# Optimization experiments

Hardware: AMD Instinct MI355X
Metric: run time of the kernel (lower is better)

## Reference

```python
import jax, jax.numpy as jnp
import numpy as np

LN_EPS = 1e-5


def setup_inputs() -> dict:
    key = jax.random.key(0)
    k1, = jax.random.split(key, 1)
    B, C, H, W = 16, 512, 64, 64
    HW = H * W
    x = jax.random.normal(k1, (B, C, H, W), dtype=jnp.float32)
    gamma = jnp.ones((), dtype=jnp.float32)          # Scale(1) learnable scalar
    ln_weight = jnp.ones((HW,), dtype=jnp.float32)   # LayerNorm weight
    ln_bias = jnp.zeros((HW,), dtype=jnp.float32)    # LayerNorm bias
    return {"x": x, "gamma": gamma, "ln_weight": ln_weight, "ln_bias": ln_bias}


def reference(x, gamma, ln_weight, ln_bias):
    B, C, H, W = x.shape
    v = x.reshape(B, C, H * W)                       # [B, C, HW] (Q = K = V)
    energy = jnp.einsum('bcn,bdn->bcd', v, v)        # [B, C, C]
    attn = jax.nn.softmax(energy, axis=-1)
    out = jnp.einsum('bcd,bdn->bcn', attn, v)        # [B, C, HW]
    out = gamma * out + v                            # scale + residual
    # LayerNorm over last dim (HW), torch eps=1e-5
    mean = jnp.mean(out, axis=-1, keepdims=True)
    var = jnp.mean(jnp.square(out - mean), axis=-1, keepdims=True)
    out = (out - mean) * jax.lax.rsqrt(var + LN_EPS) * ln_weight + ln_bias
    return out.reshape(B, C, H, W)
```

## Files before the change

### kernel.cpp

```cpp
#include <hip/hip_runtime.h>
#include <hip/hip_bf16.h>

#define B_DIM 16
#define C_DIM 512
#define HW_DIM 4096
#define LN_EPS 1e-5f

using bf16 = __hip_bfloat16;
typedef __bf16 v8bf __attribute__((ext_vector_type(8)));
typedef float v4f __attribute__((ext_vector_type(4)));
typedef unsigned short v8us __attribute__((ext_vector_type(8)));
using gptr_t = const __attribute__((address_space(1))) void*;
using lptr_t = __attribute__((address_space(3))) void*;

__device__ __forceinline__ unsigned short f2bf(float f) {
  unsigned int u = __float_as_uint(f);
  u = (u + 0x7fffu + ((u >> 16) & 1u)) >> 16;
  return (unsigned short)u;
}
__device__ __forceinline__ float bf2f(unsigned short us) {
  return __uint_as_float(((unsigned int)us) << 16);
}

__global__ __launch_bounds__(256) void k_convert_transpose(
    const float* __restrict__ x, unsigned short* __restrict__ v,
    unsigned short* __restrict__ vt) {
  __shared__ unsigned short tile[64][66];
  const int tid = threadIdx.x;
  const int b = blockIdx.z;
  const int n0 = blockIdx.x * 64;
  const int c0 = blockIdx.y * 64;
  const size_t boff = (size_t)b * ((size_t)C_DIM * HW_DIM);
  const float* xb = x + boff;
  unsigned short* vb = v + boff;
  unsigned short* vtb = vt + boff;

  const int cl = tid >> 3;
  const int h8 = (tid & 7) * 8;
#pragma unroll
  for (int j = 0; j < 2; ++j) {
    const int c = cl + j * 32;
    const float* src = xb + (size_t)(c0 + c) * HW_DIM + n0 + h8;
    const float4 f0 = ((const float4*)src)[0];
    const float4 f1 = ((const float4*)src)[1];
    v8us pack;
    pack[0] = f2bf(f0.x); pack[1] = f2bf(f0.y);
    pack[2] = f2bf(f0.z); pack[3] = f2bf(f0.w);
    pack[4] = f2bf(f1.x); pack[5] = f2bf(f1.y);
    pack[6] = f2bf(f1.z); pack[7] = f2bf(f1.w);
    *(v8us*)(vb + (size_t)(c0 + c) * HW_DIM + n0 + h8) = pack;
#pragma unroll
    for (int e = 0; e < 8; ++e) tile[c][h8 + e] = pack[e];
  }
  __syncthreads();
  const int nl = tid >> 3;
  const int c8 = (tid & 7) * 8;
#pragma unroll
  for (int j = 0; j < 2; ++j) {
    const int n = nl + j * 32;
    v8us pack;
#pragma unroll
    for (int e = 0; e < 8; ++e) pack[e] = tile[c8 + e][n];
    *(v8us*)(vtb + (size_t)(n0 + n) * C_DIM + c0 + c8) = pack;
  }
}

__device__ __forceinline__ void stage_tiles(
    const bf16* __restrict__ a_base, const bf16* __restrict__ b_base,
    const int stride, const int k0, const int wave, const int lane,
    bf16* ldsA, bf16* ldsB) {
  const int srow = lane >> 3;
  const int skcol = (lane & 7) * 8;
#pragma unroll
  for (int i = 0; i < 4; ++i) {
    const int ci = wave * 4 + i;
    const int row = ci * 8 + srow;
    __builtin_amdgcn_global_load_lds(
        (gptr_t)(a_base + (size_t)row * stride + k0 + skcol),
        (lptr_t)(ldsA + ci * 512), 16, 0, 0);
    __builtin_amdgcn_global_load_lds(
        (gptr_t)(b_base + (size_t)row * stride + k0 + skcol),
        (lptr_t)(ldsB + ci * 512), 16, 0, 0);
  }
}

__device__ __forceinline__ void compute_tile(
    const bf16* ldsA, const bf16* ldsB, const int wave, const int lane,
    v4f acc[4][4]) {
  const int kb = (lane >> 4) * 8;
  const int rl = lane & 15;
  const int wr = wave >> 1, wc = wave & 1;
#pragma unroll
  for (int kk = 0; kk < 2; ++kk) {
    v8bf af[4], bfr[4];
#pragma unroll
    for (int m = 0; m < 4; ++m)
      af[m] = *(const v8bf*)(ldsA + (wr * 64 + m * 16 + rl) * 64 + kk * 32 + kb);
#pragma unroll
    for (int n = 0; n < 4; ++n)
      bfr[n] = *(const v8bf*)(ldsB + (wc * 64 + n * 16 + rl) * 64 + kk * 32 + kb);
#pragma unroll
    for (int m = 0; m < 4; ++m)
#pragma unroll
      for (int n = 0; n < 4; ++n)
        acc[m][n] = __builtin_amdgcn_mfma_f32_16x16x32_bf16(af[m], bfr[n], acc[m][n], 0, 0, 0);
  }
}

__device__ __forceinline__ void gemm_dbuf_loop(
    const bf16* __restrict__ a_base, const bf16* __restrict__ b_base,
    const int stride, const int ksteps, const int wave, const int lane,
    bf16* ldsA0, bf16* ldsB0, bf16* ldsA1, bf16* ldsB1, v4f acc[4][4]) {
  stage_tiles(a_base, b_base, stride, 0, wave, lane, ldsA0, ldsB0);
  __syncthreads();
  int cur = 0;
  for (int kt = 0; kt < ksteps - 1; ++kt) {
    if (cur == 0)
      stage_tiles(a_base, b_base, stride, (kt + 1) * 64, wave, lane, ldsA1, ldsB1);
    else
      stage_tiles(a_base, b_base, stride, (kt + 1) * 64, wave, lane, ldsA0, ldsB0);
    compute_tile(cur == 0 ? ldsA0 : ldsA1, cur == 0 ? ldsB0 : ldsB1, wave, lane, acc);
    __syncthreads();
    cur ^= 1;
  }
  compute_tile(cur == 0 ? ldsA0 : ldsA1, cur == 0 ? ldsB0 : ldsB1, wave, lane, acc);
}

__global__ __launch_bounds__(256) void k_gemm1(
    const bf16* __restrict__ v, float* __restrict__ e_part) {
  __shared__ __align__(16) bf16 lds[4][128 * 64];
  int t = blockIdx.x;
  const int ks = t >> 8;
  t &= 255;
  const int b = t >> 4;
  const int cb = (t >> 2) & 3;
  const int db = t & 3;
  const int tid = threadIdx.x;
  const int wave = tid >> 6, lane = tid & 63;
  const bf16* vb = v + (size_t)b * ((size_t)C_DIM * HW_DIM) + ks * (HW_DIM / 2);
  v4f acc[4][4] = {};
  gemm_dbuf_loop(vb + (size_t)(cb * 128) * HW_DIM,
                 vb + (size_t)(db * 128) * HW_DIM,
                 HW_DIM, (HW_DIM / 2) / 64, wave, lane,
                 lds[0], lds[1], lds[2], lds[3], acc);
  float* eb = e_part + (size_t)ks * ((size_t)B_DIM * C_DIM * C_DIM) +
              (size_t)b * (C_DIM * C_DIM);
  const int wr = wave >> 1, wc = wave & 1;
  const int rl = lane & 15;
  const int r0 = (lane >> 4) * 4;
#pragma unroll
  for (int m = 0; m < 4; ++m)
#pragma unroll
    for (int n = 0; n < 4; ++n) {
      const int row0 = cb * 128 + wr * 64 + m * 16 + r0;
      const int col = db * 128 + wc * 64 + n * 16 + rl;
#pragma unroll
      for (int r = 0; r < 4; ++r)
        eb[(size_t)(row0 + r) * C_DIM + col] = acc[m][n][r];
    }
}

__global__ __launch_bounds__(256) void k_softmax(
    const float* __restrict__ e_part, unsigned short* __restrict__ attn) {
  const int row = blockIdx.x;
  const float* e0 = e_part + (size_t)row * C_DIM;
  const float* e1 = e0 + (size_t)B_DIM * C_DIM * C_DIM;
  const int tid = threadIdx.x;
  const float v0 = e0[tid] + e1[tid];
  const float v1 = e0[tid + 256] + e1[tid + 256];
  float mx = fmaxf(v0, v1);
#pragma unroll
  for (int off = 32; off > 0; off >>= 1) mx = fmaxf(mx, __shfl_xor(mx, off));
  __shared__ float rmax[4], rsum[4];
  const int wv = tid >> 6, ln = tid & 63;
  if (ln == 0) rmax[wv] = mx;
  __syncthreads();
  mx = fmaxf(fmaxf(rmax[0], rmax[1]), fmaxf(rmax[2], rmax[3]));
  const float p0 = __expf(v0 - mx), p1 = __expf(v1 - mx);
  float s = p0 + p1;
#pragma unroll
  for (int off = 32; off > 0; off >>= 1) s += __shfl_xor(s, off);
  if (ln == 0) rsum[wv] = s;
  __syncthreads();
  s = rsum[0] + rsum[1] + rsum[2] + rsum[3];
  const float inv = 1.0f / s;
  attn[(size_t)row * C_DIM + tid] = f2bf(p0 * inv);
  attn[(size_t)row * C_DIM + tid + 256] = f2bf(p1 * inv);
}

#define TILE_E (256 * 64)

__device__ __forceinline__ void stage_half8(
    const bf16* __restrict__ g, bf16* l, int k0, int wave, int lane) {
  const int lrow = lane >> 3, lc = lane & 7;
#pragma unroll
  for (int i = 0; i < 2; ++i) {
    const int row = i * 64 + wave * 8 + lrow;
    __builtin_amdgcn_global_load_lds(
        (gptr_t)(g + (size_t)row * C_DIM + k0 + ((lc ^ (row & 7)) << 3)),
        (lptr_t)(l + (i * 64 + wave * 8) * 64), 16, 0, 0);
  }
}
__device__ __forceinline__ void stage_op2(
    const bf16* __restrict__ g, bf16* l, int k0, int wave, int lane) {
  stage_half8(g, l, k0, wave, lane);
  stage_half8(g + (size_t)128 * C_DIM, l + 128 * 64, k0, wave, lane);
}
__device__ __forceinline__ v8bf ld_frag8(const bf16* l, int row, int j) {
  return *(const v8bf*)(l + row * 64 + ((j ^ (row & 7)) << 3));
}

__global__ __launch_bounds__(512, 2) void k_gemm2(
    const bf16* __restrict__ attn, const bf16* __restrict__ vt,
    const unsigned short* __restrict__ vres, const float* __restrict__ gamma,
    float* __restrict__ out) {
  __shared__ __align__(16) bf16 smA[2][TILE_E];
  __shared__ __align__(16) bf16 smB[2][TILE_E];
  const int bid = blockIdx.x;
  const int t = (bid & 7) * 64 + (bid >> 3);
  const int b = t >> 5;
  const int cb = (t >> 4) & 1;
  const int nb = t & 15;
  const int tid = threadIdx.x;
  const int wave = tid >> 6, lane = tid & 63;
  const int wm = wave >> 2, wn = wave & 3;
  const int rl = lane & 15, kq = lane >> 4;

  const bf16* Ab = attn + (size_t)b * (C_DIM * C_DIM) + (size_t)(cb * 256) * C_DIM;
  const bf16* Bb = vt + (size_t)b * ((size_t)C_DIM * HW_DIM) + (size_t)(nb * 256) * C_DIM;

  v4f acc[8][4] = {};

  stage_op2(Bb, smB[0], 0, wave, lane);
  stage_op2(Ab, smA[0], 0, wave, lane);
  stage_op2(Bb, smB[1], 64, wave, lane);
  stage_op2(Ab, smA[1], 64, wave, lane);
  asm volatile("s_waitcnt vmcnt(8)" ::: "memory");
  __builtin_amdgcn_s_barrier();

  v8bf a[4][2], b01[2][2], b23[2][2];
  for (int kt = 0; kt < 8; ++kt) {
    const bf16* LA = smA[kt & 1];
    const bf16* LB = smB[kt & 1];
#pragma unroll
    for (int mi = 0; mi < 4; ++mi)
#pragma unroll
      for (int kk = 0; kk < 2; ++kk)
        a[mi][kk] = ld_frag8(LA, wm * 128 + mi * 16 + rl, kk * 4 + kq);
#pragma unroll
    for (int ni = 0; ni < 2; ++ni)
#pragma unroll
      for (int kk = 0; kk < 2; ++kk)
        b01[ni][kk] = ld_frag8(LB, wn * 64 + ni * 16 + rl, kk * 4 + kq);
    __builtin_amdgcn_s_barrier();
    asm volatile("s_waitcnt lgkmcnt(0)");
    __builtin_amdgcn_s_setprio(1);
#pragma unroll
    for (int kk = 0; kk < 2; ++kk)
#pragma unroll
      for (int mi = 0; mi < 4; ++mi)
#pragma unroll
        for (int ni = 0; ni < 2; ++ni)
          acc[mi][ni] = __builtin_amdgcn_mfma_f32_16x16x32_bf16(
              a[mi][kk], b01[ni][kk], acc[mi][ni], 0, 0, 0);
    __builtin_amdgcn_s_setprio(0);
    __builtin_amdgcn_s_barrier();
#pragma unroll
    for (int ni = 0; ni < 2; ++ni)
#pragma unroll
      for (int kk = 0; kk < 2; ++kk)
        b23[ni][kk] = ld_frag8(LB, wn * 64 + (ni + 2) * 16 + rl, kk * 4 + kq);
    __builtin_amdgcn_s_barrier();
    asm volatile("s_waitcnt lgkmcnt(0)");
    __builtin_amdgcn_s_setprio(1);
#pragma unroll
    for (int kk = 0; kk < 2; ++kk)
#pragma unroll
      for (int mi = 0; mi < 4; ++mi)
#pragma unroll
        for (int ni = 0; ni < 2; ++ni)
          acc[mi][ni + 2] = __builtin_amdgcn_mfma_f32_16x16x32_bf16(
              a[mi][kk], b23[ni][kk], acc[mi][ni + 2], 0, 0, 0);
    __builtin_amdgcn_s_setprio(0);
    __builtin_amdgcn_s_barrier();
#pragma unroll
    for (int mi = 0; mi < 4; ++mi)
#pragma unroll
      for (int kk = 0; kk < 2; ++kk)
        a[mi][kk] = ld_frag8(LA, wm * 128 + (mi + 4) * 16 + rl, kk * 4 + kq);
    if (kt < 6) stage_op2(Bb, smB[kt & 1], (kt + 2) * 64, wave, lane);
    __builtin_amdgcn_s_barrier();
    asm volatile("s_waitcnt lgkmcnt(0)");
    __builtin_amdgcn_s_setprio(1);
#pragma unroll
    for (int kk = 0; kk < 2; ++kk)
#pragma unroll
      for (int mi = 0; mi < 4; ++mi)
#pragma unroll
        for (int ni = 0; ni < 2; ++ni)
          acc[mi + 4][ni + 2] = __builtin_amdgcn_mfma_f32_16x16x32_bf16(
              a[mi][kk], b23[ni][kk], acc[mi + 4][ni + 2], 0, 0, 0);
    __builtin_amdgcn_s_setprio(0);
    __builtin_amdgcn_s_barrier();
    if (kt < 6) stage_op2(Ab, smA[kt & 1], (kt + 2) * 64, wave, lane);
    __builtin_amdgcn_s_barrier();
    __builtin_amdgcn_s_setprio(1);
#pragma unroll
    for (int kk = 0; kk < 2; ++kk)
#pragma unroll
      for (int mi = 0; mi < 4; ++mi)
#pragma unroll
        for (int ni = 0; ni < 2; ++ni)
          acc[mi + 4][ni] = __builtin_amdgcn_mfma_f32_16x16x32_bf16(
              a[mi][kk], b01[ni][kk], acc[mi + 4][ni], 0, 0, 0);
    __builtin_amdgcn_s_setprio(0);
    if (kt < 6)
      asm volatile("s_waitcnt vmcnt(8)" ::: "memory");
    else if (kt == 6)
      asm volatile("s_waitcnt vmcnt(0)" ::: "memory");
    __builtin_amdgcn_s_barrier();
  }

  const float g = gamma[0];
  const size_t boff = (size_t)b * ((size_t)C_DIM * HW_DIM);
  const unsigned short* xb = vres + boff;
  float* ob = out + boff;
  const int r0 = kq * 4;
#pragma unroll
  for (int mi = 0; mi < 8; ++mi)
#pragma unroll
    for (int ni = 0; ni < 4; ++ni) {
      const int c0 = cb * 256 + wm * 128 + mi * 16 + r0;
      const int nn = nb * 256 + wn * 64 + ni * 16 + rl;
#pragma unroll
      for (int r = 0; r < 4; ++r) {
        const size_t idx = (size_t)(c0 + r) * HW_DIM + nn;
        ob[idx] = g * acc[mi][ni][r] + bf2f(xb[idx]);
      }
    }
}

__global__ __launch_bounds__(256) void k_ln(
    float* __restrict__ out, const float* __restrict__ w,
    const float* __restrict__ bias) {
  const int row = blockIdx.x;
  float* p = out + (size_t)row * HW_DIM;
  const int tid = threadIdx.x;
  float4 vals[4];
  float s = 0.f, ss = 0.f;
#pragma unroll
  for (int i = 0; i < 4; ++i) {
    const float4 vv = ((const float4*)p)[tid + i * 256];
    vals[i] = vv;
    s += vv.x + vv.y + vv.z + vv.w;
    ss += vv.x * vv.x + vv.y * vv.y + vv.z * vv.z + vv.w * vv.w;
  }
#pragma unroll
  for (int off = 32; off > 0; off >>= 1) {
    s += __shfl_xor(s, off);
    ss += __shfl_xor(ss, off);
  }
  __shared__ float rs[4], rss[4];
  const int wv = tid >> 6, ln = tid & 63;
  if (ln == 0) { rs[wv] = s; rss[wv] = ss; }
  __syncthreads();
  s = rs[0] + rs[1] + rs[2] + rs[3];
  ss = rss[0] + rss[1] + rss[2] + rss[3];
  const float mean = s * (1.f / HW_DIM);
  const float var = ss * (1.f / HW_DIM) - mean * mean;
  const float rstd = rsqrtf(var + LN_EPS);
#pragma unroll
  for (int i = 0; i < 4; ++i) {
    const int idx = tid + i * 256;
    const float4 vv = vals[i];
    const float4 w4 = ((const float4*)w)[idx];
    const float4 b4 = ((const float4*)bias)[idx];
    float4 r;
    r.x = (vv.x - mean) * rstd * w4.x + b4.x;
    r.y = (vv.y - mean) * rstd * w4.y + b4.y;
    r.z = (vv.z - mean) * rstd * w4.z + b4.z;
    r.w = (vv.w - mean) * rstd * w4.w + b4.w;
    ((float4*)p)[idx] = r;
  }
}

extern "C" void kernel_launch(void* const* d_in, const int* in_sizes, int n_in,
                              void* d_out, int out_size, void* d_ws, size_t ws_size,
                              hipStream_t stream) {
  const float* x = (const float*)d_in[0];
  const float* gamma = (const float*)d_in[1];
  const float* lnw = (const float*)d_in[2];
  const float* lnb = (const float*)d_in[3];
  float* out = (float*)d_out;
  char* ws = (char*)d_ws;

  const size_t n_elem = (size_t)B_DIM * C_DIM * HW_DIM;
  const size_t e_elems = (size_t)B_DIM * C_DIM * C_DIM;
  unsigned short* vbf = (unsigned short*)ws;
  unsigned short* vbfT = (unsigned short*)(ws + 2 * n_elem);
  float* e_part = (float*)(ws + 4 * n_elem);
  unsigned short* attn =
      (unsigned short*)(ws + 4 * n_elem + 2 * e_elems * sizeof(float));

  k_convert_transpose<<<dim3(HW_DIM / 64, C_DIM / 64, B_DIM), 256, 0, stream>>>(
      x, vbf, vbfT);
  k_gemm1<<<512, 256, 0, stream>>>((const bf16*)vbf, e_part);
  k_softmax<<<B_DIM * C_DIM, 256, 0, stream>>>(e_part, attn);
  k_gemm2<<<512, 512, 0, stream>>>((const bf16*)attn, (const bf16*)vbfT,
                                   vbf, gamma, out);
  k_ln<<<B_DIM * C_DIM, 256, 0, stream>>>(out, lnw, lnb);
}
```

Measured before the change: 231.0 us.

## Stage GEMM2 epilogue through LDS for coalesced stores; move residual into LayerNorm

The GEMM2 epilogue now writes accumulators into a merged, XOR-swizzled shared buffer in two halves, then writes full rows back with float4 coalesced stores instead of scattered scalar stores. The gamma scaling and bf16 residual add move from GEMM2 into the LayerNorm kernel, which already reads each row. This targets poor store coalescing in GEMM2 and removes its strided residual reads. The cost is extra barriers and LDS traffic in the epilogue, plus an extra bf16 read stream in LayerNorm.

```diff
diff --git a/kernel.cpp b/kernel.cpp
--- a/kernel.cpp
+++ b/kernel.cpp
@@ -10,6 +10,7 @@
 typedef __bf16 v8bf __attribute__((ext_vector_type(8)));
 typedef float v4f __attribute__((ext_vector_type(4)));
 typedef unsigned short v8us __attribute__((ext_vector_type(8)));
+typedef unsigned short v4us __attribute__((ext_vector_type(4)));
 using gptr_t = const __attribute__((address_space(1))) void*;
 using lptr_t = __attribute__((address_space(3))) void*;
 
@@ -212,10 +213,8 @@
 
 __global__ __launch_bounds__(512, 2) void k_gemm2(
     const bf16* __restrict__ attn, const bf16* __restrict__ vt,
-    const unsigned short* __restrict__ vres, const float* __restrict__ gamma,
     float* __restrict__ out) {
-  __shared__ __align__(16) bf16 smA[2][TILE_E];
-  __shared__ __align__(16) bf16 smB[2][TILE_E];
+  __shared__ __align__(16) bf16 smem[4 * TILE_E];
   const int bid = blockIdx.x;
   const int t = (bid & 7) * 64 + (bid >> 3);
   const int b = t >> 5;
@@ -231,17 +230,19 @@
 
   v4f acc[8][4] = {};
 
-  stage_op2(Bb, smB[0], 0, wave, lane);
-  stage_op2(Ab, smA[0], 0, wave, lane);
-  stage_op2(Bb, smB[1], 64, wave, lane);
-  stage_op2(Ab, smA[1], 64, wave, lane);
+  stage_op2(Bb, smem + 2 * TILE_E, 0, wave, lane);
+  stage_op2(Ab, smem, 0, wave, lane);
+  stage_op2(Bb, smem + 3 * TILE_E, 64, wave, lane);
+  stage_op2(Ab, smem + TILE_E, 64, wave, lane);
   asm volatile("s_waitcnt vmcnt(8)" ::: "memory");
   __builtin_amdgcn_s_barrier();
 
   v8bf a[4][2], b01[2][2], b23[2][2];
   for (int kt = 0; kt < 8; ++kt) {
-    const bf16* LA = smA[kt & 1];
-    const bf16* LB = smB[kt & 1];
+    const bf16* LA = smem + (kt & 1) * TILE_E;
+    const bf16* LB = smem + (2 + (kt & 1)) * TILE_E;
+    bf16* SA = smem + (kt & 1) * TILE_E;
+    bf16* SB = smem + (2 + (kt & 1)) * TILE_E;
 #pragma unroll
     for (int mi = 0; mi < 4; ++mi)
 #pragma unroll
@@ -288,7 +289,7 @@
 #pragma unroll
       for (int kk = 0; kk < 2; ++kk)
         a[mi][kk] = ld_frag8(LA, wm * 128 + (mi + 4) * 16 + rl, kk * 4 + kq);
-    if (kt < 6) stage_op2(Bb, smB[kt & 1], (kt + 2) * 64, wave, lane);
+    if (kt < 6) stage_op2(Bb, SB, (kt + 2) * 64, wave, lane);
     __builtin_amdgcn_s_barrier();
     asm volatile("s_waitcnt lgkmcnt(0)");
     __builtin_amdgcn_s_setprio(1);
@@ -302,7 +303,7 @@
               a[mi][kk], b23[ni][kk], acc[mi + 4][ni + 2], 0, 0, 0);
     __builtin_amdgcn_s_setprio(0);
     __builtin_amdgcn_s_barrier();
-    if (kt < 6) stage_op2(Ab, smA[kt & 1], (kt + 2) * 64, wave, lane);
+    if (kt < 6) stage_op2(Ab, SA, (kt + 2) * 64, wave, lane);
     __builtin_amdgcn_s_barrier();
     __builtin_amdgcn_s_setprio(1);
 #pragma unroll
@@ -321,36 +322,58 @@
     __builtin_amdgcn_s_barrier();
   }
 
-  const float g = gamma[0];
-  const size_t boff = (size_t)b * ((size_t)C_DIM * HW_DIM);
-  const unsigned short* xb = vres + boff;
-  float* ob = out + boff;
-  const int r0 = kq * 4;
-#pragma unroll
-  for (int mi = 0; mi < 8; ++mi)
-#pragma unroll
-    for (int ni = 0; ni < 4; ++ni) {
-      const int c0 = cb * 256 + wm * 128 + mi * 16 + r0;
-      const int nn = nb * 256 + wn * 64 + ni * 16 + rl;
-#pragma unroll
-      for (int r = 0; r < 4; ++r) {
-        const size_t idx = (size_t)(c0 + r) * HW_DIM + nn;
-        ob[idx] = g * acc[mi][ni][r] + bf2f(xb[idx]);
-      }
+  float* smf = (float*)smem;
+  float* ob = out + (size_t)b * ((size_t)C_DIM * HW_DIM) +
+              (size_t)(cb * 256) * HW_DIM + nb * 256;
+#pragma unroll
+  for (int h = 0; h < 2; ++h) {
+    if (wm == h) {
+#pragma unroll
+      for (int mi = 0; mi < 8; ++mi)
+#pragma unroll
+        for (int ni = 0; ni < 4; ++ni)
+#pragma unroll
+          for (int rr = 0; rr < 4; ++rr) {
+            const int rloc = mi * 16 + kq * 4 + rr;
+            const int col = wn * 64 + ni * 16 + rl;
+            const int key = rloc & 7;
+            smf[rloc * 256 + ((((col >> 2) ^ key) << 2) | (col & 3))] =
+                acc[mi][ni][rr];
+          }
     }
+    __syncthreads();
+#pragma unroll
+    for (int it = 0; it < 16; ++it) {
+      const int rloc = it * 8 + wave;
+      const float4 vv =
+          *(const float4*)(smf + rloc * 256 + ((lane ^ (rloc & 7)) << 2));
+      *(float4*)(ob + (size_t)(h * 128 + rloc) * HW_DIM + lane * 4) = vv;
+    }
+    __syncthreads();
+  }
 }
 
 __global__ __launch_bounds__(256) void k_ln(
-    float* __restrict__ out, const float* __restrict__ w,
+    float* __restrict__ out, const unsigned short* __restrict__ vres,
+    const float* __restrict__ gamma, const float* __restrict__ w,
     const float* __restrict__ bias) {
   const int row = blockIdx.x;
   float* p = out + (size_t)row * HW_DIM;
+  const unsigned short* vr = vres + (size_t)row * HW_DIM;
+  const float g = gamma[0];
   const int tid = threadIdx.x;
   float4 vals[4];
   float s = 0.f, ss = 0.f;
 #pragma unroll
   for (int i = 0; i < 4; ++i) {
-    const float4 vv = ((const float4*)p)[tid + i * 256];
+    const int idx = tid + i * 256;
+    const float4 av = ((const float4*)p)[idx];
+    const v4us rv = *(const v4us*)(vr + idx * 4);
+    float4 vv;
+    vv.x = g * av.x + bf2f(rv[0]);
+    vv.y = g * av.y + bf2f(rv[1]);
+    vv.z = g * av.z + bf2f(rv[2]);
+    vv.w = g * av.w + bf2f(rv[3]);
     vals[i] = vv;
     s += vv.x + vv.y + vv.z + vv.w;
     ss += vv.x * vv.x + vv.y * vv.y + vv.z * vv.z + vv.w * vv.w;
@@ -406,7 +429,6 @@
       x, vbf, vbfT);
   k_gemm1<<<512, 256, 0, stream>>>((const bf16*)vbf, e_part);
   k_softmax<<<B_DIM * C_DIM, 256, 0, stream>>>(e_part, attn);
-  k_gemm2<<<512, 512, 0, stream>>>((const bf16*)attn, (const bf16*)vbfT,
-                                   vbf, gamma, out);
-  k_ln<<<B_DIM * C_DIM, 256, 0, stream>>>(out, lnw, lnb);
-}
+  k_gemm2<<<512, 512, 0, stream>>>((const bf16*)attn, (const bf16*)vbfT, out);
+  k_ln<<<B_DIM * C_DIM, 256, 0, stream>>>(out, vbf, gamma, lnw, lnb);
+}
```

After: 231.8 us. About the same (+0.3%).
